# Kernel optimization log

Measured on AMD Instinct MI355X. Metric: run time of the kernel, lower is better.

## Reference

```python
import jax, jax.numpy as jnp
import numpy as np

HEADS = 8
WINDOW = 16

def _pointwise(W, b, t):
    # Conv1d(C, C, kernel=1): (B, C, T) -> (B, C, T)
    return jnp.einsum('oc,bct->bot', W, t) + b[None, :, None]

def setup_inputs() -> dict:
    key = jax.random.key(0)
    ks = jax.random.split(key, 10)
    B, C, T = 4, 512, 4096
    s = 0.02
    return {
        'x':    jax.random.normal(ks[0], (B, C, T), jnp.float32),
        'cond': jax.random.normal(ks[1], (B, C, T), jnp.float32),
        'Wq': jax.random.normal(ks[2], (C, C), jnp.float32) * s,
        'bq': jnp.zeros((C,), jnp.float32),
        'Wk': jax.random.normal(ks[3], (C, C), jnp.float32) * s,
        'bk': jnp.zeros((C,), jnp.float32),
        'Wv': jax.random.normal(ks[4], (C, C), jnp.float32) * s,
        'bv': jnp.zeros((C,), jnp.float32),
        'Wo': jax.random.normal(ks[5], (C, C), jnp.float32) * s,
        'bo': jnp.zeros((C,), jnp.float32),
    }

def reference(x, cond, Wq, bq, Wk, bk, Wv, bv, Wo, bo):
    B, C, T = x.shape
    H, W = HEADS, WINDOW
    hd = C // H
    scale = hd ** (-0.5)
    pad_left = W // 2          # 8
    pad_right = W - pad_left - 1  # 7

    q = _pointwise(Wq, bq, x)      # (B, C, T)
    k = _pointwise(Wk, bk, cond)
    v = _pointwise(Wv, bv, cond)

    k = jnp.pad(k, ((0, 0), (0, 0), (pad_left, pad_right)))  # (B, C, T+W-1)
    v = jnp.pad(v, ((0, 0), (0, 0), (pad_left, pad_right)))

    # sliding windows of size W, stride 1 -> T_unf == T
    idx = jnp.arange(T)[:, None] + jnp.arange(W)[None, :]  # (T, W)
    k_win = k[:, :, idx].reshape(B, H, hd, T, W)
    v_win = v[:, :, idx].reshape(B, H, hd, T, W)
    qh = q.reshape(B, H, hd, T)

    dots = jnp.einsum('bhdt,bhdtw->bhtw', qh, k_win) * scale
    attn = jax.nn.softmax(dots, axis=-1)
    out = jnp.einsum('bhtw,bhdtw->bhdt', attn, v_win)  # (B, H, hd, T)
    out = out.reshape(B, C, T)
    return _pointwise(Wo, bo, out)
```

## Files before the change

### kernel.cpp

```cpp
#include <hip/hip_runtime.h>

#define CC 512
#define TT 4096
#define NB 4
#define NH 8
#define HD 64

typedef __attribute__((ext_vector_type(8))) short s16x8;
typedef __attribute__((ext_vector_type(4))) float f32x4;
typedef __attribute__((ext_vector_type(4))) unsigned int u32x4;

#if defined(__has_builtin)
#  if __has_builtin(__builtin_amdgcn_fdot2_f32_bf16)
#    define HAS_BF16_DOT2 1
#  else
#    define HAS_BF16_DOT2 0
#  endif
#else
#  define HAS_BF16_DOT2 0
#endif

__device__ __forceinline__ short f2bf(float f) {
    unsigned u = __float_as_uint(f);
    unsigned r = (u + 0x7fffu + ((u >> 16) & 1u)) >> 16;
    return (short)r;
}
__device__ __forceinline__ float bf2f(short s) {
    return __uint_as_float(((unsigned)(unsigned short)s) << 16);
}

#if HAS_BF16_DOT2
typedef __attribute__((ext_vector_type(2))) __bf16 bf16x2;
__device__ __forceinline__ float dot2bf(unsigned a, unsigned b, float c) {
    return __builtin_amdgcn_fdot2_f32_bf16(__builtin_bit_cast(bf16x2, a),
                                           __builtin_bit_cast(bf16x2, b), c, false);
}
#else
__device__ __forceinline__ float dot2bf(unsigned a, unsigned b, float c) {
    float r = fmaf(bf2f((short)(a & 0xffffu)), bf2f((short)(b & 0xffffu)), c);
    return fmaf(bf2f((short)(a >> 16)), bf2f((short)(b >> 16)), r);
}
#endif

__device__ __forceinline__ void gld_lds16(const void* g, void* s) {
    __builtin_amdgcn_global_load_lds(
        (const __attribute__((address_space(1))) unsigned int*)g,
        (__attribute__((address_space(3))) unsigned int*)s, 16, 0, 0);
}

__global__ __launch_bounds__(256) void cvt_w_k(const float* __restrict__ w0,
                                               const float* __restrict__ w1,
                                               const float* __restrict__ w2,
                                               const float* __restrict__ w3,
                                               short* __restrict__ dst) {
    int i = blockIdx.x * 256 + threadIdx.x;
    const float* s = (i < 262144) ? w0 : (i < 524288) ? w1 : (i < 786432) ? w2 : w3;
    dst[i] = f2bf(s[i & 262143]);
}

__global__ __launch_bounds__(256) void trans_k(const float* __restrict__ x,
                                               const float* __restrict__ cond,
                                               short* __restrict__ xT,
                                               short* __restrict__ condT) {
    __shared__ float tile[64][65];
    int z = blockIdx.z;
    int b = z & 3;
    const float* src = (z < 4 ? x : cond) + (size_t)b * CC * TT;
    short* dst = (z < 4 ? xT : condT) + (size_t)b * TT * CC;
    int tx = threadIdx.x & 63, ty = threadIdx.x >> 6;
    int t0 = blockIdx.x * 64, c0 = blockIdx.y * 64;
#pragma unroll
    for (int r = 0; r < 64; r += 4)
        tile[ty + r][tx] = src[(size_t)(c0 + ty + r) * TT + t0 + tx];
    __syncthreads();
#pragma unroll
    for (int r = 0; r < 64; r += 4)
        dst[(size_t)(t0 + ty + r) * CC + c0 + tx] = f2bf(tile[tx][ty + r]);
}

template <int TMAJOR>
__device__ __forceinline__ void gemm128(const short* __restrict__ Wm,
                                        const short* __restrict__ Sm,
                                        const float* __restrict__ bias,
                                        float* __restrict__ Df,
                                        short* __restrict__ Db) {
    __shared__ short Al[128 * 64] __attribute__((aligned(16)));
    __shared__ short Bl[128 * 64] __attribute__((aligned(16)));
    const int tid = threadIdx.x;
    const int lane = tid & 63;
    const int wid = tid >> 6;
    const int o0 = blockIdx.y * 128;
    const int t0 = blockIdx.x * 128;
    const int wm = (wid >> 1) * 64;
    const int wn = (wid & 1) * 64;

    f32x4 acc[4][4];
#pragma unroll
    for (int i = 0; i < 4; i++)
#pragma unroll
        for (int j = 0; j < 4; j++) acc[i][j] = (f32x4){0.f, 0.f, 0.f, 0.f};

    const int cbase = (wid * 4) << 6;

    for (int kt = 0; kt < 8; ++kt) {
        const int k0 = kt * 64;
        __syncthreads();
#pragma unroll
        for (int j = 0; j < 4; ++j) {
            int c = cbase + (j << 6) + lane;
            int m = c >> 3, kc = c & 7;
            int kcs = kc ^ (m & 7);
            gld_lds16(Wm + (size_t)(o0 + m) * CC + k0 + kcs * 8,
                      &Al[(cbase + (j << 6)) << 3]);
            gld_lds16(Sm + (size_t)(t0 + m) * CC + k0 + kcs * 8,
                      &Bl[(cbase + (j << 6)) << 3]);
        }
        __syncthreads();
#pragma unroll
        for (int kk = 0; kk < 2; ++kk) {
            const int kb = kk * 32 + (lane >> 4) * 8;
            s16x8 af[4], bfr[4];
#pragma unroll
            for (int i = 0; i < 4; i++) {
                int m = wm + i * 16 + (lane & 15);
                af[i] = *(const s16x8*)&Al[(m * 64 + kb) ^ ((m & 7) << 3)];
                int n = wn + i * 16 + (lane & 15);
                bfr[i] = *(const s16x8*)&Bl[(n * 64 + kb) ^ ((n & 7) << 3)];
            }
#pragma unroll
            for (int mi = 0; mi < 4; mi++)
#pragma unroll
                for (int ni = 0; ni < 4; ni++) {
                    if (TMAJOR)
                        acc[mi][ni] = __builtin_amdgcn_mfma_f32_16x16x32_bf16(
                            bfr[mi], af[ni], acc[mi][ni], 0, 0, 0);
                    else
                        acc[mi][ni] = __builtin_amdgcn_mfma_f32_16x16x32_bf16(
                            af[mi], bfr[ni], acc[mi][ni], 0, 0, 0);
                }
        }
    }

    const int col = lane & 15;
    const int rg = (lane >> 4) << 2;
    if (TMAJOR) {
#pragma unroll
        for (int ti = 0; ti < 4; ti++) {
            int t = t0 + wn + ti * 16 + rg;
#pragma unroll
            for (int oi = 0; oi < 4; oi++) {
                int o = o0 + wm + oi * 16 + col;
                float bv = bias[o];
                f32x4 a = acc[ti][oi];
#pragma unroll
                for (int r = 0; r < 4; r++)
                    Db[(size_t)(t + r) * CC + o] = f2bf(a[r] + bv);
            }
        }
    } else {
#pragma unroll
        for (int mi = 0; mi < 4; mi++) {
            int o = o0 + wm + mi * 16 + rg;
#pragma unroll
            for (int ni = 0; ni < 4; ni++) {
                int t = t0 + wn + ni * 16 + col;
                f32x4 a = acc[mi][ni];
#pragma unroll
                for (int r = 0; r < 4; r++)
                    Df[(size_t)(o + r) * TT + t] = a[r] + bias[o + r];
            }
        }
    }
}

__global__ __launch_bounds__(256, 2) void gemm_qkv_k(
    const short* __restrict__ Wb, const short* __restrict__ xT,
    const short* __restrict__ condT, const float* __restrict__ bq,
    const float* __restrict__ bk, const float* __restrict__ bv,
    short* __restrict__ qkvT) {
    int z = blockIdx.z, which = z >> 2, b = z & 3;
    const short* Wm = Wb + (size_t)which * CC * CC;
    const short* Sm = (which == 0 ? xT : condT) + (size_t)b * TT * CC;
    const float* bias = which == 0 ? bq : (which == 1 ? bk : bv);
    short* Db = qkvT + ((size_t)which * NB + b) * TT * CC;
    gemm128<1>(Wm, Sm, bias, nullptr, Db);
}

__global__ __launch_bounds__(256, 2) void gemm_o_k(const short* __restrict__ Wb,
                                                   const short* __restrict__ outT,
                                                   const float* __restrict__ bo,
                                                   float* __restrict__ out) {
    int b = blockIdx.z;
    gemm128<0>(Wb + 3 * (size_t)CC * CC, outT + (size_t)b * TT * CC, bo,
               out + (size_t)b * CC * TT, nullptr);
}

__global__ __launch_bounds__(64, 4) void attn5_k(const short* __restrict__ qkvT,
                                                 short* __restrict__ outT) {
    __shared__ unsigned kl[640 * 4] __attribute__((aligned(16)));
    __shared__ unsigned vl[640 * 4] __attribute__((aligned(16)));
    const int lane = threadIdx.x;
    const int t0 = blockIdx.x * 64;
    const int h = blockIdx.y, b = blockIdx.z;
    const size_t BTC = (size_t)NB * TT * CC;
    const short* qg = qkvT + (size_t)b * TT * CC + h * HD;
    const short* kg = qg + BTC;
    const short* vg = qg + 2 * BTC;

#pragma unroll
    for (int it = 0; it < 10; ++it) {
        int idx = it * 64 + lane;
        int row = idx >> 3, s = idx & 7;
        int c = s ^ (row & 7);
        int t = t0 - 8 + row;
        t = t < 0 ? 0 : (t > TT - 1 ? TT - 1 : t);
        const size_t off = (size_t)t * CC + c * 8;
        gld_lds16(kg + off, &kl[it * 256]);
        gld_lds16(vg + off, &vl[it * 256]);
    }

    u32x4 qv[8];
    {
        const u32x4* qr = (const u32x4*)(qg + (size_t)(t0 + lane) * CC);
#pragma unroll
        for (int c = 0; c < 8; ++c) qv[c] = qr[c];
    }

    __syncthreads();

    float dots[16];
#pragma unroll
    for (int w = 0; w < 16; ++w) {
        const int row = lane + w;
        float a0 = 0.f, a1 = 0.f, a2 = 0.f, a3 = 0.f;
#pragma unroll
        for (int c = 0; c < 8; ++c) {
            u32x4 kc = *(const u32x4*)&kl[(row * 8 + (c ^ (row & 7))) * 4];
            a0 = dot2bf(qv[c][0], kc[0], a0);
            a1 = dot2bf(qv[c][1], kc[1], a1);
            a2 = dot2bf(qv[c][2], kc[2], a2);
            a3 = dot2bf(qv[c][3], kc[3], a3);
        }
        int s = t0 - 8 + row;
        dots[w] = ((unsigned)s < (unsigned)TT) ? ((a0 + a1) + (a2 + a3)) * 0.125f
                                               : 0.f;
    }

    unsigned pp[8];
    {
        float mx = dots[0];
#pragma unroll
        for (int w = 1; w < 16; ++w) mx = fmaxf(mx, dots[w]);
        float e[16], sum = 0.f;
#pragma unroll
        for (int w = 0; w < 16; ++w) {
            e[w] = __expf(dots[w] - mx);
            sum += e[w];
        }
        const float inv = 1.f / sum;
        const int sb = t0 - 8 + lane;
#pragma unroll
        for (int i = 0; i < 8; ++i) {
            float p0 = ((unsigned)(sb + 2 * i) < (unsigned)TT) ? e[2 * i] * inv : 0.f;
            float p1 = ((unsigned)(sb + 2 * i + 1) < (unsigned)TT) ? e[2 * i + 1] * inv : 0.f;
            pp[i] = (unsigned)(unsigned short)f2bf(p0) |
                    ((unsigned)(unsigned short)f2bf(p1) << 16);
        }
    }

    short* ob = outT + ((size_t)b * TT + t0 + lane) * CC + h * HD;
#pragma unroll
    for (int half = 0; half < 2; ++half) {
        float of[32];
#pragma unroll
        for (int j = 0; j < 32; ++j) of[j] = 0.f;
#pragma unroll
        for (int i = 0; i < 8; ++i) {
            const int r0 = lane + 2 * i, r1 = r0 + 1;
#pragma unroll
            for (int cl = 0; cl < 4; ++cl) {
                const int c = half * 4 + cl;
                u32x4 va = *(const u32x4*)&vl[(r0 * 8 + (c ^ (r0 & 7))) * 4];
                u32x4 vb = *(const u32x4*)&vl[(r1 * 8 + (c ^ (r1 & 7))) * 4];
#pragma unroll
                for (int d = 0; d < 4; ++d) {
                    unsigned lo = __builtin_amdgcn_perm(vb[d], va[d], 0x05040100u);
                    unsigned hi = __builtin_amdgcn_perm(vb[d], va[d], 0x07060302u);
                    of[cl * 8 + 2 * d]     = dot2bf(pp[i], lo, of[cl * 8 + 2 * d]);
                    of[cl * 8 + 2 * d + 1] = dot2bf(pp[i], hi, of[cl * 8 + 2 * d + 1]);
                }
            }
        }
#pragma unroll
        for (int cl = 0; cl < 4; ++cl) {
            s16x8 pk;
#pragma unroll
            for (int j = 0; j < 8; ++j) pk[j] = f2bf(of[cl * 8 + j]);
            *(s16x8*)&ob[half * 32 + cl * 8] = pk;
        }
    }
}

extern "C" void kernel_launch(void* const* d_in, const int* in_sizes, int n_in,
                              void* d_out, int out_size, void* d_ws, size_t ws_size,
                              hipStream_t stream) {
    const float* x    = (const float*)d_in[0];
    const float* cond = (const float*)d_in[1];
    const float* Wq   = (const float*)d_in[2];
    const float* bq   = (const float*)d_in[3];
    const float* Wk   = (const float*)d_in[4];
    const float* bk   = (const float*)d_in[5];
    const float* Wv   = (const float*)d_in[6];
    const float* bv   = (const float*)d_in[7];
    const float* Wo   = (const float*)d_in[8];
    const float* bo   = (const float*)d_in[9];

    char* ws = (char*)d_ws;
    short* Wb    = (short*)ws;
    short* xT    = (short*)(ws + (2u << 20));
    short* condT = (short*)(ws + (18u << 20));
    short* qkvT  = (short*)(ws + (34u << 20));
    short* outT  = xT;

    cvt_w_k<<<4096, 256, 0, stream>>>(Wq, Wk, Wv, Wo, Wb);
    trans_k<<<dim3(TT / 64, CC / 64, 8), 256, 0, stream>>>(x, cond, xT, condT);
    gemm_qkv_k<<<dim3(TT / 128, CC / 128, 12), 256, 0, stream>>>(Wb, xT, condT, bq, bk, bv, qkvT);
    attn5_k<<<dim3(TT / 64, NH, NB), 64, 0, stream>>>(qkvT, outT);
    gemm_o_k<<<dim3(TT / 128, CC / 128, 4), 256, 0, stream>>>(Wb, outT, bo, (float*)d_out);
}
```

Measured before the change: 90.43 us.

## Split attention head dimension across half-waves with cross-lane reduction of dots

The attention kernel now processes 32 timesteps per block instead of 64. The two half-waves each handle one 32-wide half of the head dimension, and their partial QK dot products are combined with a cross-lane shuffle before the softmax. This doubles the block count and halves per-thread register and LDS footprint, aiming for more parallelism and occupancy in the attention stage. In exchange, the softmax is computed redundantly in both halves, a shuffle is added, and each block loads a larger share of halo K/V rows (48 rows per 32 outputs).

After: 93.77 us. 3.7% more time.

```diff
diff --git a/kernel.cpp b/kernel.cpp
--- a/kernel.cpp
+++ b/kernel.cpp
@@ -195,12 +195,14 @@
                out + (size_t)b * CC * TT, nullptr);
 }
 
-__global__ __launch_bounds__(64, 4) void attn5_k(const short* __restrict__ qkvT,
+__global__ __launch_bounds__(64, 4) void attn7_k(const short* __restrict__ qkvT,
                                                  short* __restrict__ outT) {
-    __shared__ unsigned kl[640 * 4] __attribute__((aligned(16)));
-    __shared__ unsigned vl[640 * 4] __attribute__((aligned(16)));
+    __shared__ unsigned kl[384 * 4] __attribute__((aligned(16)));
+    __shared__ unsigned vl[384 * 4] __attribute__((aligned(16)));
     const int lane = threadIdx.x;
-    const int t0 = blockIdx.x * 64;
+    const int tl = lane & 31;
+    const int dh = lane >> 5;
+    const int t0 = blockIdx.x * 32;
     const int h = blockIdx.y, b = blockIdx.z;
     const size_t BTC = (size_t)NB * TT * CC;
     const short* qg = qkvT + (size_t)b * TT * CC + h * HD;
@@ -208,7 +210,7 @@
     const short* vg = qg + 2 * BTC;
 
 #pragma unroll
-    for (int it = 0; it < 10; ++it) {
+    for (int it = 0; it < 6; ++it) {
         int idx = it * 64 + lane;
         int row = idx >> 3, s = idx & 7;
         int c = s ^ (row & 7);
@@ -219,11 +221,11 @@
         gld_lds16(vg + off, &vl[it * 256]);
     }
 
-    u32x4 qv[8];
+    u32x4 qv[4];
     {
-        const u32x4* qr = (const u32x4*)(qg + (size_t)(t0 + lane) * CC);
-#pragma unroll
-        for (int c = 0; c < 8; ++c) qv[c] = qr[c];
+        const u32x4* qr = (const u32x4*)(qg + (size_t)(t0 + tl) * CC + dh * 32);
+#pragma unroll
+        for (int c = 0; c < 4; ++c) qv[c] = qr[c];
     }
 
     __syncthreads();
@@ -231,19 +233,24 @@
     float dots[16];
 #pragma unroll
     for (int w = 0; w < 16; ++w) {
-        const int row = lane + w;
+        const int row = tl + w;
         float a0 = 0.f, a1 = 0.f, a2 = 0.f, a3 = 0.f;
 #pragma unroll
-        for (int c = 0; c < 8; ++c) {
+        for (int cc = 0; cc < 4; ++cc) {
+            const int c = dh * 4 + cc;
             u32x4 kc = *(const u32x4*)&kl[(row * 8 + (c ^ (row & 7))) * 4];
-            a0 = dot2bf(qv[c][0], kc[0], a0);
-            a1 = dot2bf(qv[c][1], kc[1], a1);
-            a2 = dot2bf(qv[c][2], kc[2], a2);
-            a3 = dot2bf(qv[c][3], kc[3], a3);
-        }
-        int s = t0 - 8 + row;
-        dots[w] = ((unsigned)s < (unsigned)TT) ? ((a0 + a1) + (a2 + a3)) * 0.125f
-                                               : 0.f;
+            a0 = dot2bf(qv[cc][0], kc[0], a0);
+            a1 = dot2bf(qv[cc][1], kc[1], a1);
+            a2 = dot2bf(qv[cc][2], kc[2], a2);
+            a3 = dot2bf(qv[cc][3], kc[3], a3);
+        }
+        dots[w] = (a0 + a1) + (a2 + a3);
+    }
+#pragma unroll
+    for (int w = 0; w < 16; ++w) {
+        float full = dots[w] + __shfl_xor(dots[w], 32);
+        int s = t0 - 8 + tl + w;
+        dots[w] = ((unsigned)s < (unsigned)TT) ? full * 0.125f : 0.f;
     }
 
     unsigned pp[8];
@@ -258,7 +265,7 @@
             sum += e[w];
         }
         const float inv = 1.f / sum;
-        const int sb = t0 - 8 + lane;
+        const int sb = t0 - 8 + tl;
 #pragma unroll
         for (int i = 0; i < 8; ++i) {
             float p0 = ((unsigned)(sb + 2 * i) < (unsigned)TT) ? e[2 * i] * inv : 0.f;
@@ -268,36 +275,33 @@
         }
     }
 
-    short* ob = outT + ((size_t)b * TT + t0 + lane) * CC + h * HD;
-#pragma unroll
-    for (int half = 0; half < 2; ++half) {
-        float of[32];
-#pragma unroll
-        for (int j = 0; j < 32; ++j) of[j] = 0.f;
-#pragma unroll
-        for (int i = 0; i < 8; ++i) {
-            const int r0 = lane + 2 * i, r1 = r0 + 1;
-#pragma unroll
-            for (int cl = 0; cl < 4; ++cl) {
-                const int c = half * 4 + cl;
-                u32x4 va = *(const u32x4*)&vl[(r0 * 8 + (c ^ (r0 & 7))) * 4];
-                u32x4 vb = *(const u32x4*)&vl[(r1 * 8 + (c ^ (r1 & 7))) * 4];
-#pragma unroll
-                for (int d = 0; d < 4; ++d) {
-                    unsigned lo = __builtin_amdgcn_perm(vb[d], va[d], 0x05040100u);
-                    unsigned hi = __builtin_amdgcn_perm(vb[d], va[d], 0x07060302u);
-                    of[cl * 8 + 2 * d]     = dot2bf(pp[i], lo, of[cl * 8 + 2 * d]);
-                    of[cl * 8 + 2 * d + 1] = dot2bf(pp[i], hi, of[cl * 8 + 2 * d + 1]);
-                }
+    float of[32];
+#pragma unroll
+    for (int j = 0; j < 32; ++j) of[j] = 0.f;
+#pragma unroll
+    for (int i = 0; i < 8; ++i) {
+        const int r0 = tl + 2 * i, r1 = r0 + 1;
+#pragma unroll
+        for (int cc = 0; cc < 4; ++cc) {
+            const int c = dh * 4 + cc;
+            u32x4 va = *(const u32x4*)&vl[(r0 * 8 + (c ^ (r0 & 7))) * 4];
+            u32x4 vb = *(const u32x4*)&vl[(r1 * 8 + (c ^ (r1 & 7))) * 4];
+#pragma unroll
+            for (int d = 0; d < 4; ++d) {
+                unsigned lo = __builtin_amdgcn_perm(vb[d], va[d], 0x05040100u);
+                unsigned hi = __builtin_amdgcn_perm(vb[d], va[d], 0x07060302u);
+                of[cc * 8 + 2 * d]     = dot2bf(pp[i], lo, of[cc * 8 + 2 * d]);
+                of[cc * 8 + 2 * d + 1] = dot2bf(pp[i], hi, of[cc * 8 + 2 * d + 1]);
             }
         }
-#pragma unroll
-        for (int cl = 0; cl < 4; ++cl) {
-            s16x8 pk;
-#pragma unroll
-            for (int j = 0; j < 8; ++j) pk[j] = f2bf(of[cl * 8 + j]);
-            *(s16x8*)&ob[half * 32 + cl * 8] = pk;
-        }
+    }
+    short* ob = outT + ((size_t)b * TT + t0 + tl) * CC + h * HD + dh * 32;
+#pragma unroll
+    for (int cc = 0; cc < 4; ++cc) {
+        s16x8 pk;
+#pragma unroll
+        for (int j = 0; j < 8; ++j) pk[j] = f2bf(of[cc * 8 + j]);
+        *(s16x8*)&ob[cc * 8] = pk;
     }
 }
 
@@ -325,6 +329,6 @@
     cvt_w_k<<<4096, 256, 0, stream>>>(Wq, Wk, Wv, Wo, Wb);
     trans_k<<<dim3(TT / 64, CC / 64, 8), 256, 0, stream>>>(x, cond, xT, condT);
     gemm_qkv_k<<<dim3(TT / 128, CC / 128, 12), 256, 0, stream>>>(Wb, xT, condT, bq, bk, bv, qkvT);
-    attn5_k<<<dim3(TT / 64, NH, NB), 64, 0, stream>>>(qkvT, outT);
+    attn7_k<<<dim3(TT / 32, NH, NB), 64, 0, stream>>>(qkvT, outT);
     gemm_o_k<<<dim3(TT / 128, CC / 128, 4), 256, 0, stream>>>(Wb, outT, bo, (float*)d_out);
 }
```

## Fuse K and V projections into one GEMM sharing the cond tile

Applied to the files above, without the earlier changes.

Splits the combined QKV projection launch into a Q-only GEMM and a fused K/V GEMM. The K/V kernel loads each condT tile into shared memory once and feeds it to two accumulator sets, one for Wk and one for Wv, which halves reads of the cond activations. The cost is doubled accumulator registers (32 f32x4 per thread) under a 256x2 launch bound, which risks spills or lower occupancy. It also adds an extra kernel launch and produces fewer blocks for the K/V part.

Result: slower. 96.62 us (+6.9%).

```diff
diff --git a/kernel.cpp b/kernel.cpp
--- a/kernel.cpp
+++ b/kernel.cpp
@@ -173,17 +173,104 @@
     }
 }
 
-__global__ __launch_bounds__(256, 2) void gemm_qkv_k(
+__global__ __launch_bounds__(256, 2) void gemm_q_k(
     const short* __restrict__ Wb, const short* __restrict__ xT,
-    const short* __restrict__ condT, const float* __restrict__ bq,
+    const float* __restrict__ bq, short* __restrict__ qkvT) {
+    int b = blockIdx.z;
+    gemm128<1>(Wb, xT + (size_t)b * TT * CC, bq, nullptr,
+               qkvT + (size_t)b * TT * CC);
+}
+
+__global__ __launch_bounds__(256, 2) void gemm_kv_k(
+    const short* __restrict__ Wb, const short* __restrict__ condT,
     const float* __restrict__ bk, const float* __restrict__ bv,
     short* __restrict__ qkvT) {
-    int z = blockIdx.z, which = z >> 2, b = z & 3;
-    const short* Wm = Wb + (size_t)which * CC * CC;
-    const short* Sm = (which == 0 ? xT : condT) + (size_t)b * TT * CC;
-    const float* bias = which == 0 ? bq : (which == 1 ? bk : bv);
-    short* Db = qkvT + ((size_t)which * NB + b) * TT * CC;
-    gemm128<1>(Wm, Sm, bias, nullptr, Db);
+    __shared__ short Akl[128 * 64] __attribute__((aligned(16)));
+    __shared__ short Avl[128 * 64] __attribute__((aligned(16)));
+    __shared__ short Bl[128 * 64] __attribute__((aligned(16)));
+    const int b = blockIdx.z;
+    const short* Wk_m = Wb + (size_t)1 * CC * CC;
+    const short* Wv_m = Wb + (size_t)2 * CC * CC;
+    const short* Sm = condT + (size_t)b * TT * CC;
+    short* Dk = qkvT + ((size_t)1 * NB + b) * TT * CC;
+    short* Dv = qkvT + ((size_t)2 * NB + b) * TT * CC;
+
+    const int tid = threadIdx.x;
+    const int lane = tid & 63;
+    const int wid = tid >> 6;
+    const int o0 = blockIdx.y * 128;
+    const int t0 = blockIdx.x * 128;
+    const int wm = (wid >> 1) * 64;
+    const int wn = (wid & 1) * 64;
+
+    f32x4 acck[4][4], accv[4][4];
+#pragma unroll
+    for (int i = 0; i < 4; i++)
+#pragma unroll
+        for (int j = 0; j < 4; j++) {
+            acck[i][j] = (f32x4){0.f, 0.f, 0.f, 0.f};
+            accv[i][j] = (f32x4){0.f, 0.f, 0.f, 0.f};
+        }
+
+    const int cbase = (wid * 4) << 6;
+
+    for (int kt = 0; kt < 8; ++kt) {
+        const int k0 = kt * 64;
+        __syncthreads();
+#pragma unroll
+        for (int j = 0; j < 4; ++j) {
+            int c = cbase + (j << 6) + lane;
+            int m = c >> 3, kc = c & 7;
+            int kcs = kc ^ (m & 7);
+            const size_t roff = (size_t)(o0 + m) * CC + k0 + kcs * 8;
+            const int dst = (cbase + (j << 6)) << 3;
+            gld_lds16(Wk_m + roff, &Akl[dst]);
+            gld_lds16(Wv_m + roff, &Avl[dst]);
+            gld_lds16(Sm + (size_t)(t0 + m) * CC + k0 + kcs * 8, &Bl[dst]);
+        }
+        __syncthreads();
+#pragma unroll
+        for (int kk = 0; kk < 2; ++kk) {
+            const int kb = kk * 32 + (lane >> 4) * 8;
+            s16x8 afk[4], afv[4], bfr[4];
+#pragma unroll
+            for (int i = 0; i < 4; i++) {
+                int m = wm + i * 16 + (lane & 15);
+                int ao = (m * 64 + kb) ^ ((m & 7) << 3);
+                afk[i] = *(const s16x8*)&Akl[ao];
+                afv[i] = *(const s16x8*)&Avl[ao];
+                int n = wn + i * 16 + (lane & 15);
+                bfr[i] = *(const s16x8*)&Bl[(n * 64 + kb) ^ ((n & 7) << 3)];
+            }
+#pragma unroll
+            for (int mi = 0; mi < 4; mi++)
+#pragma unroll
+                for (int ni = 0; ni < 4; ni++) {
+                    acck[mi][ni] = __builtin_amdgcn_mfma_f32_16x16x32_bf16(
+                        bfr[mi], afk[ni], acck[mi][ni], 0, 0, 0);
+                    accv[mi][ni] = __builtin_amdgcn_mfma_f32_16x16x32_bf16(
+                        bfr[mi], afv[ni], accv[mi][ni], 0, 0, 0);
+                }
+        }
+    }
+
+    const int col = lane & 15;
+    const int rg = (lane >> 4) << 2;
+#pragma unroll
+    for (int ti = 0; ti < 4; ti++) {
+        int t = t0 + wn + ti * 16 + rg;
+#pragma unroll
+        for (int oi = 0; oi < 4; oi++) {
+            int o = o0 + wm + oi * 16 + col;
+            float bkv = bk[o], bvv = bv[o];
+            f32x4 ak = acck[ti][oi], av = accv[ti][oi];
+#pragma unroll
+            for (int r = 0; r < 4; r++) {
+                Dk[(size_t)(t + r) * CC + o] = f2bf(ak[r] + bkv);
+                Dv[(size_t)(t + r) * CC + o] = f2bf(av[r] + bvv);
+            }
+        }
+    }
 }
 
 __global__ __launch_bounds__(256, 2) void gemm_o_k(const short* __restrict__ Wb,
@@ -324,7 +411,8 @@
 
     cvt_w_k<<<4096, 256, 0, stream>>>(Wq, Wk, Wv, Wo, Wb);
     trans_k<<<dim3(TT / 64, CC / 64, 8), 256, 0, stream>>>(x, cond, xT, condT);
-    gemm_qkv_k<<<dim3(TT / 128, CC / 128, 12), 256, 0, stream>>>(Wb, xT, condT, bq, bk, bv, qkvT);
+    gemm_q_k<<<dim3(TT / 128, CC / 128, NB), 256, 0, stream>>>(Wb, xT, bq, qkvT);
+    gemm_kv_k<<<dim3(TT / 128, CC / 128, NB), 256, 0, stream>>>(Wb, condT, bk, bv, qkvT);
     attn5_k<<<dim3(TT / 64, NH, NB), 64, 0, stream>>>(qkvT, outT);
-    gemm_o_k<<<dim3(TT / 128, CC / 128, 4), 256, 0, stream>>>(Wb, outT, bo, (float*)d_out);
-}
+    gemm_o_k<<<dim3(TT / 128, CC / 128, NB), 256, 0, stream>>>(Wb, outT, bo, (float*)d_out);
+}
```

## Replace QKV GEMM with 256x256 double-buffered 8-wave pipelined kernel

Applied to the files above, without the earlier changes.

Swaps the QKV projection GEMM for a new kernel with 256x256 tiles, 512 threads and double-buffered LDS. Global-to-LDS loads for the next K step are split into quarter stages interleaved with MFMA quadrants, using explicit vmcnt waits, barriers and s_setprio. The aim is to overlap memory traffic with matrix math and raise data reuse per block. In exchange it uses 128KB of LDS per block, launches only 384 blocks, and depends on fragile hand-written wait counts.

After: 102.3 us. 13.1% more time.

```diff
diff --git a/kernel.cpp b/kernel.cpp
--- a/kernel.cpp
+++ b/kernel.cpp
@@ -78,12 +78,152 @@
         dst[(size_t)(t0 + ty + r) * CC + c0 + tx] = f2bf(tile[tx][ty + r]);
 }
 
-template <int TMAJOR>
-__device__ __forceinline__ void gemm128(const short* __restrict__ Wm,
-                                        const short* __restrict__ Sm,
-                                        const float* __restrict__ bias,
-                                        float* __restrict__ Df,
-                                        short* __restrict__ Db) {
+__global__ __launch_bounds__(512, 2) void gemm_qkv8_k(
+    const short* __restrict__ Wb, const short* __restrict__ xT,
+    const short* __restrict__ condT, const float* __restrict__ bq,
+    const float* __restrict__ bk, const float* __restrict__ bv,
+    short* __restrict__ qkvT) {
+    __shared__ short Sl[2][256 * 64] __attribute__((aligned(16)));
+    __shared__ short Wl[2][256 * 64] __attribute__((aligned(16)));
+    const int z = blockIdx.z, which = z >> 2, b = z & 3;
+    const short* Wm = Wb + (size_t)which * CC * CC;
+    const short* Sm = (which == 0 ? xT : condT) + (size_t)b * TT * CC;
+    const float* bias = which == 0 ? bq : (which == 1 ? bk : bv);
+    short* Db = qkvT + ((size_t)which * NB + b) * TT * CC;
+
+    const int tid = threadIdx.x;
+    const int lane = tid & 63, wid = tid >> 6;
+    const int wr = wid >> 2;
+    const int wc = wid & 3;
+    const int t0 = blockIdx.x * 256;
+    const int o0 = blockIdx.y * 256;
+    const short* SA = Sm + (size_t)t0 * CC;
+    const short* WA = Wm + (size_t)o0 * CC;
+
+#define STAGE(MAT, SRC, HALF, BUF, K0)                                        \
+    {                                                                         \
+        _Pragma("unroll") for (int l = 0; l < 2; ++l) {                       \
+            int idx2 = l * 512 + tid;                                         \
+            int row = (HALF)*128 + (idx2 >> 3), sl_ = idx2 & 7;               \
+            int c = sl_ ^ (row & 7);                                          \
+            gld_lds16(SRC + (size_t)row * CC + (K0) + c * 8,                  \
+                      &MAT[BUF][((HALF)*1024 + idx2) * 8]);                   \
+        }                                                                     \
+    }
+
+#define READ_A(MH, BUF)                                                       \
+    _Pragma("unroll") for (int kk = 0; kk < 2; ++kk)                          \
+    _Pragma("unroll") for (int mi = 0; mi < 4; ++mi) {                        \
+        int R = (MH)*128 + wr * 64 + mi * 16 + (lane & 15);                   \
+        int g = kk * 4 + (lane >> 4);                                         \
+        a[kk][mi] = *(const s16x8*)&Sl[BUF][(R * 8 + (g ^ (R & 7))) * 8];     \
+    }
+
+#define READ_B(NH, BUF)                                                       \
+    _Pragma("unroll") for (int kk = 0; kk < 2; ++kk)                          \
+    _Pragma("unroll") for (int ni = 0; ni < 2; ++ni) {                        \
+        int R = (NH)*128 + wc * 32 + ni * 16 + (lane & 15);                   \
+        int g = kk * 4 + (lane >> 4);                                         \
+        bb[kk][ni] = *(const s16x8*)&Wl[BUF][(R * 8 + (g ^ (R & 7))) * 8];    \
+    }
+
+#define MFMA_Q(MH, NH)                                                        \
+    __builtin_amdgcn_s_setprio(1);                                            \
+    _Pragma("unroll") for (int mi = 0; mi < 4; ++mi)                          \
+    _Pragma("unroll") for (int ni = 0; ni < 2; ++ni)                          \
+    _Pragma("unroll") for (int kk = 0; kk < 2; ++kk)                          \
+        acc[MH][mi][NH][ni] = __builtin_amdgcn_mfma_f32_16x16x32_bf16(        \
+            a[kk][mi], bb[kk][ni], acc[MH][mi][NH][ni], 0, 0, 0);             \
+    __builtin_amdgcn_s_setprio(0);
+
+#define BAR()                       \
+    __builtin_amdgcn_s_barrier();   \
+    __builtin_amdgcn_sched_barrier(0);
+
+    f32x4 acc[2][4][2][2];
+#pragma unroll
+    for (int i = 0; i < 2; i++)
+#pragma unroll
+        for (int j = 0; j < 4; j++)
+#pragma unroll
+            for (int k = 0; k < 2; k++)
+#pragma unroll
+                for (int l = 0; l < 2; l++) acc[i][j][k][l] = (f32x4){0.f, 0.f, 0.f, 0.f};
+    s16x8 a[2][4];
+    s16x8 bb[2][2];
+
+    STAGE(Sl, SA, 0, 0, 0);
+    STAGE(Wl, WA, 0, 0, 0);
+    STAGE(Wl, WA, 1, 0, 0);
+    STAGE(Sl, SA, 1, 0, 0);
+    asm volatile("s_waitcnt vmcnt(4)" ::: "memory");
+    BAR();
+
+    for (int kt = 0; kt < 8; ++kt) {
+        const int buf = kt & 1, nbuf = buf ^ 1;
+        const int kn = (kt + 1) * 64;
+        if (kt < 7) {
+            STAGE(Sl, SA, 0, nbuf, kn);
+            asm volatile("s_waitcnt vmcnt(4)" ::: "memory");
+        } else {
+            asm volatile("s_waitcnt vmcnt(2)" ::: "memory");
+        }
+        BAR();
+        READ_A(0, buf);
+        READ_B(0, buf);
+        MFMA_Q(0, 0);
+        if (kt < 7) {
+            STAGE(Wl, WA, 0, nbuf, kn);
+            asm volatile("s_waitcnt vmcnt(4)" ::: "memory");
+        } else {
+            asm volatile("s_waitcnt vmcnt(0)" ::: "memory");
+        }
+        BAR();
+        READ_B(1, buf);
+        MFMA_Q(0, 1);
+        if (kt < 7) STAGE(Wl, WA, 1, nbuf, kn);
+        BAR();
+        READ_A(1, buf);
+        MFMA_Q(1, 1);
+        if (kt < 7) {
+            STAGE(Sl, SA, 1, nbuf, kn);
+            asm volatile("s_waitcnt vmcnt(4)" ::: "memory");
+        }
+        BAR();
+        READ_B(0, buf);
+        MFMA_Q(1, 0);
+    }
+#undef STAGE
+#undef READ_A
+#undef READ_B
+#undef MFMA_Q
+#undef BAR
+
+    const int col = lane & 15;
+    const int rg = (lane >> 4) << 2;
+#pragma unroll
+    for (int mh = 0; mh < 2; ++mh)
+#pragma unroll
+        for (int mi = 0; mi < 4; ++mi) {
+            int t = t0 + mh * 128 + wr * 64 + mi * 16 + rg;
+#pragma unroll
+            for (int nh = 0; nh < 2; ++nh)
+#pragma unroll
+                for (int ni = 0; ni < 2; ++ni) {
+                    int o = o0 + nh * 128 + wc * 32 + ni * 16 + col;
+                    float bv = bias[o];
+                    f32x4 v = acc[mh][mi][nh][ni];
+#pragma unroll
+                    for (int r = 0; r < 4; r++)
+                        Db[(size_t)(t + r) * CC + o] = f2bf(v[r] + bv);
+                }
+        }
+}
+
+__device__ __forceinline__ void gemm128_o(const short* __restrict__ Wm,
+                                          const short* __restrict__ Sm,
+                                          const float* __restrict__ bias,
+                                          float* __restrict__ Df) {
     __shared__ short Al[128 * 64] __attribute__((aligned(16)));
     __shared__ short Bl[128 * 64] __attribute__((aligned(16)));
     const int tid = threadIdx.x;
@@ -130,60 +270,26 @@
 #pragma unroll
             for (int mi = 0; mi < 4; mi++)
 #pragma unroll
-                for (int ni = 0; ni < 4; ni++) {
-                    if (TMAJOR)
-                        acc[mi][ni] = __builtin_amdgcn_mfma_f32_16x16x32_bf16(
-                            bfr[mi], af[ni], acc[mi][ni], 0, 0, 0);
-                    else
-                        acc[mi][ni] = __builtin_amdgcn_mfma_f32_16x16x32_bf16(
-                            af[mi], bfr[ni], acc[mi][ni], 0, 0, 0);
-                }
+                for (int ni = 0; ni < 4; ni++)
+                    acc[mi][ni] = __builtin_amdgcn_mfma_f32_16x16x32_bf16(
+                        af[mi], bfr[ni], acc[mi][ni], 0, 0, 0);
         }
     }
 
     const int col = lane & 15;
     const int rg = (lane >> 4) << 2;
-    if (TMAJOR) {
-#pragma unroll
-        for (int ti = 0; ti < 4; ti++) {
-            int t = t0 + wn + ti * 16 + rg;
-#pragma unroll
-            for (int oi = 0; oi < 4; oi++) {
-                int o = o0 + wm + oi * 16 + col;
-                float bv = bias[o];
-                f32x4 a = acc[ti][oi];
-#pragma unroll
-                for (int r = 0; r < 4; r++)
-                    Db[(size_t)(t + r) * CC + o] = f2bf(a[r] + bv);
-            }
-        }
-    } else {
-#pragma unroll
-        for (int mi = 0; mi < 4; mi++) {
-            int o = o0 + wm + mi * 16 + rg;
-#pragma unroll
-            for (int ni = 0; ni < 4; ni++) {
-                int t = t0 + wn + ni * 16 + col;
-                f32x4 a = acc[mi][ni];
-#pragma unroll
-                for (int r = 0; r < 4; r++)
-                    Df[(size_t)(o + r) * TT + t] = a[r] + bias[o + r];
-            }
-        }
-    }
-}
-
-__global__ __launch_bounds__(256, 2) void gemm_qkv_k(
-    const short* __restrict__ Wb, const short* __restrict__ xT,
-    const short* __restrict__ condT, const float* __restrict__ bq,
-    const float* __restrict__ bk, const float* __restrict__ bv,
-    short* __restrict__ qkvT) {
-    int z = blockIdx.z, which = z >> 2, b = z & 3;
-    const short* Wm = Wb + (size_t)which * CC * CC;
-    const short* Sm = (which == 0 ? xT : condT) + (size_t)b * TT * CC;
-    const float* bias = which == 0 ? bq : (which == 1 ? bk : bv);
-    short* Db = qkvT + ((size_t)which * NB + b) * TT * CC;
-    gemm128<1>(Wm, Sm, bias, nullptr, Db);
+#pragma unroll
+    for (int mi = 0; mi < 4; mi++) {
+        int o = o0 + wm + mi * 16 + rg;
+#pragma unroll
+        for (int ni = 0; ni < 4; ni++) {
+            int t = t0 + wn + ni * 16 + col;
+            f32x4 v = acc[mi][ni];
+#pragma unroll
+            for (int r = 0; r < 4; r++)
+                Df[(size_t)(o + r) * TT + t] = v[r] + bias[o + r];
+        }
+    }
 }
 
 __global__ __launch_bounds__(256, 2) void gemm_o_k(const short* __restrict__ Wb,
@@ -191,8 +297,8 @@
                                                    const float* __restrict__ bo,
                                                    float* __restrict__ out) {
     int b = blockIdx.z;
-    gemm128<0>(Wb + 3 * (size_t)CC * CC, outT + (size_t)b * TT * CC, bo,
-               out + (size_t)b * CC * TT, nullptr);
+    gemm128_o(Wb + 3 * (size_t)CC * CC, outT + (size_t)b * TT * CC, bo,
+              out + (size_t)b * CC * TT);
 }
 
 __global__ __launch_bounds__(64, 4) void attn5_k(const short* __restrict__ qkvT,
@@ -324,7 +430,7 @@
 
     cvt_w_k<<<4096, 256, 0, stream>>>(Wq, Wk, Wv, Wo, Wb);
     trans_k<<<dim3(TT / 64, CC / 64, 8), 256, 0, stream>>>(x, cond, xT, condT);
-    gemm_qkv_k<<<dim3(TT / 128, CC / 128, 12), 256, 0, stream>>>(Wb, xT, condT, bq, bk, bv, qkvT);
+    gemm_qkv8_k<<<dim3(TT / 256, CC / 256, 12), 512, 0, stream>>>(Wb, xT, condT, bq, bk, bv, qkvT);
     attn5_k<<<dim3(TT / 64, NH, NB), 64, 0, stream>>>(qkvT, outT);
-    gemm_o_k<<<dim3(TT / 128, CC / 128, 4), 256, 0, stream>>>(Wb, outT, bo, (float*)d_out);
-}
+    gemm_o_k<<<dim3(TT / 128, CC / 128, NB), 256, 0, stream>>>(Wb, outT, bo, (float*)d_out);
+}
```
